# Performance work log

Measured on AMD Instinct MI355X. Metric: run time of the kernel, lower is better.

## Reference

```python
import jax, jax.numpy as jnp
import numpy as np

# ViT-Base-ish encoder: 256x256 img, patch 8 -> N=1024 tokens, dim 768, 8 layers
B, C, H, W = 8, 3, 256, 256
P, D, DEPTH, HEADS, DH, MLP = 8, 768, 8, 12, 64, 3072
N = (H // P) * (W // P)
INNER = HEADS * DH  # 768
EPS = 1e-5


def setup_inputs() -> dict:
    key = jax.random.key(0)
    ks = jax.random.split(key, 8)
    s = lambda i, shape, scale=0.02: jax.random.normal(ks[i], shape, jnp.float32) * scale
    return {
        "x": s(0, (B, C, H, W), 1.0),
        "w_conv": s(1, (D, C, P, P)),          # OIHW conv kernel (patch embed)
        "b_conv": jnp.zeros((D,), jnp.float32),
        "pos_emb": s(2, (1, N, D)),
        "ln1_w": jnp.ones((DEPTH, D), jnp.float32),
        "ln1_b": jnp.zeros((DEPTH, D), jnp.float32),
        "qkv_w": s(3, (DEPTH, D, 3 * INNER)),  # stored [in,out]; Linear has no bias
        "out_w": s(4, (DEPTH, INNER, D)),
        "out_b": jnp.zeros((DEPTH, D), jnp.float32),
        "ln2_w": jnp.ones((DEPTH, D), jnp.float32),
        "ln2_b": jnp.zeros((DEPTH, D), jnp.float32),
        "w1": s(5, (DEPTH, D, MLP)),
        "b1": jnp.zeros((DEPTH, MLP), jnp.float32),
        "w2": s(6, (DEPTH, MLP, D)),
        "b2": jnp.zeros((DEPTH, D), jnp.float32),
    }


def _layernorm(x, w, b):
    m = jnp.mean(x, axis=-1, keepdims=True)
    v = jnp.mean(jnp.square(x - m), axis=-1, keepdims=True)
    return (x - m) * jax.lax.rsqrt(v + EPS) * w + b


def _encoder(x, w_conv, b_conv, pos_emb, ln1_w, ln1_b, qkv_w, out_w, out_b,
             ln2_w, ln2_b, w1, b1, w2, b2):
    # PatchEmbed: strided conv -> flatten(2).transpose(1,2)
    h = jax.lax.conv_general_dilated(
        x, w_conv, window_strides=(P, P), padding='VALID',
        dimension_numbers=('NCHW', 'OIHW', 'NCHW'))
    h = h + b_conv[None, :, None, None]
    h = h.reshape(B, D, N).transpose(0, 2, 1)  # [B, N, D]
    h = h + pos_emb
    scale = DH ** -0.5

    def block(h, p):
        l1w, l1b, qkvw, ow, ob, l2w, l2b, W1, B1, W2, B2 = p
        # PreNorm + MHSA
        y = _layernorm(h, l1w, l1b)
        qkv = y @ qkvw                                   # [B,N,3*INNER]
        q, k, v = jnp.split(qkv, 3, axis=-1)
        split_heads = lambda t: t.reshape(B, N, HEADS, DH).transpose(0, 2, 1, 3)
        q, k, v = split_heads(q), split_heads(k), split_heads(v)
        attn = jax.nn.softmax(jnp.einsum('bhnd,bhmd->bhnm', q, k) * scale, axis=-1)
        o = jnp.einsum('bhnm,bhmd->bhnd', attn, v)
        o = o.transpose(0, 2, 1, 3).reshape(B, N, INNER)
        h = h + (o @ ow + ob)
        # PreNorm + FFN (exact GELU, dropout=0)
        y = _layernorm(h, l2w, l2b)
        h = h + (jax.nn.gelu(y @ W1 + B1, approximate=False) @ W2 + B2)
        return h, None

    h, _ = jax.lax.scan(block, h, (ln1_w, ln1_b, qkv_w, out_w, out_b,
                                   ln2_w, ln2_b, w1, b1, w2, b2))
    return h


def reference(x, w_conv, b_conv, pos_emb, ln1_w, ln1_b, qkv_w, out_w, out_b,
              ln2_w, ln2_b, w1, b1, w2, b2):
    return _encoder(x, w_conv, b_conv, pos_emb, ln1_w, ln1_b, qkv_w, out_w,
                    out_b, ln2_w, ln2_b, w1, b1, w2, b2)
```

## Files before the change

kernel.cpp:

```cpp
#include <hip/hip_runtime.h>
#include <math.h>

#define BATCH 8
#define CIN 3
#define HIMG 256
#define WIMG 256
#define PATCH 8
#define DMODEL 768
#define DEPTH 8
#define HEADS 12
#define DHEAD 64
#define MLPDIM 3072
#define NTOK 1024
#define INNER 768
#define MROWS (BATCH * NTOK)
#define QKVS (3 * INNER)
#define KPATCH (CIN * PATCH * PATCH)
#define LNEPS 1e-5f
#define QSCALE 0.18033688011112042f

typedef __attribute__((ext_vector_type(8))) short short8;
typedef __attribute__((ext_vector_type(4))) float v4f;

__device__ __forceinline__ float b2f(unsigned short u) {
  union { unsigned int i; float f; } x;
  x.i = (unsigned int)u << 16;
  return x.f;
}
__device__ __forceinline__ unsigned short f2b(float f) {
  union { float f; unsigned int i; } x;
  x.f = f;
  unsigned int r = x.i + 0x7FFFu + ((x.i >> 16) & 1u);
  return (unsigned short)(r >> 16);
}
__device__ __forceinline__ unsigned int pkrh(float a, float b) {
  union { float f; unsigned int u; } x, y;
  x.f = a; y.f = b;
  return ((x.u + 0x8000u) >> 16) | ((y.u + 0x8000u) & 0xFFFF0000u);
}

#define GLL(gp, lp)                                                     \
  __builtin_amdgcn_global_load_lds(                                     \
      (const __attribute__((address_space(1))) void*)(gp),              \
      (__attribute__((address_space(3))) void*)(lp), 16, 0, 0)

__global__ __launch_bounds__(256) void cast_kernel(
    const float* __restrict__ src, unsigned short* __restrict__ dst, int n) {
  int i = blockIdx.x * 256 + threadIdx.x;
  if (i < n) dst[i] = f2b(src[i]);
}

__global__ __launch_bounds__(256) void transpose_cast_kernel(
    const float* __restrict__ src, unsigned short* __restrict__ dst, int R,
    int C) {
  __shared__ unsigned short t[32][33];
  src += (size_t)blockIdx.z * R * C;
  dst += (size_t)blockIdx.z * R * C;
  int c0 = blockIdx.x * 32, r0 = blockIdx.y * 32;
  int tx = threadIdx.x & 31, ty = threadIdx.x >> 5;
#pragma unroll
  for (int u = 0; u < 4; ++u) {
    int r = r0 + ty + u * 8;
    t[ty + u * 8][tx] = f2b(src[(size_t)r * C + c0 + tx]);
  }
  __syncthreads();
#pragma unroll
  for (int u = 0; u < 4; ++u) {
    int c = c0 + ty + u * 8;
    dst[(size_t)c * R + r0 + tx] = t[tx][ty + u * 8];
  }
}

__global__ __launch_bounds__(256) void vtrans_kernel(
    const unsigned short* __restrict__ qkv, unsigned short* __restrict__ vt) {
  __shared__ unsigned short t[32][33];
  int k0 = blockIdx.x * 32;
  int d0 = blockIdx.y * 32;
  int bh = blockIdx.z;
  int b = bh / HEADS, h = bh % HEADS;
  int tx = threadIdx.x & 31, ty = threadIdx.x >> 5;
  const unsigned short* src =
      qkv + (size_t)(b * NTOK) * QKVS + 2 * INNER + h * DHEAD;
#pragma unroll
  for (int u = 0; u < 4; ++u)
    t[ty + u * 8][tx] = src[(size_t)(k0 + ty + u * 8) * QKVS + d0 + tx];
  __syncthreads();
  unsigned short* dst = vt + ((size_t)bh * DHEAD + d0) * NTOK + k0;
#pragma unroll
  for (int u = 0; u < 4; ++u)
    dst[(size_t)(ty + u * 8) * NTOK + tx] = t[tx][ty + u * 8];
}

__global__ __launch_bounds__(256) void im2col_kernel(
    const float* __restrict__ x, unsigned short* __restrict__ A) {
  int idx = blockIdx.x * 256 + threadIdx.x;
  if (idx >= MROWS * KPATCH) return;
  int m = idx / KPATCH, k = idx % KPATCH;
  int b = m / NTOK, n = m % NTOK;
  int ph = n / 32, pw = n % 32;
  int c = k / 64, r = k % 64;
  int py = r / 8, px = r % 8;
  A[idx] =
      f2b(x[((size_t)(b * CIN + c) * HIMG + ph * 8 + py) * WIMG + pw * 8 + px]);
}

template <int EPI, int OB, int MT>
__global__ __launch_bounds__(256) void mfma_gemm_kernel(
    const unsigned short* __restrict__ Ag, const unsigned short* __restrict__ Bt,
    const float* __restrict__ bias, const float* __restrict__ res,
    void* __restrict__ Cg, int Mdim, int Ndim, int Kdim) {
  constexpr int MI = MT / 32;
  constexpr int RA = MT / 4;
  constexpr int NCA = RA / 8;
  __shared__ __align__(16) unsigned short Asm[MT * 64];
  __shared__ __align__(16) unsigned short Bsm[128 * 64];
  int tid = threadIdx.x;
  int lane = tid & 63, wv = tid >> 6;

  int Nt = Ndim / 128;
  int mchunk = (Mdim / MT) >> 3;
  int bid = blockIdx.x;
  int xcd = bid & 7;
  int j = bid >> 3;
  int m0 = (xcd * mchunk + j / Nt) * MT;
  int n0 = (j % Nt) * 128;

  v4f acc[MI][4] = {};

  int sr8 = lane >> 3;
  int sc8 = ((lane & 7) ^ sr8) * 8;
  const unsigned short* Aw = Ag + (size_t)(m0 + RA * wv + sr8) * Kdim + sc8;
  const unsigned short* Bw = Bt + (size_t)(n0 + 32 * wv + sr8) * Kdim + sc8;
  unsigned short* As0 = Asm + (RA * wv) * 64;
  unsigned short* Bs0 = Bsm + (32 * wv) * 64;

  int quad = lane >> 4, lr = lane & 15;
  int fr0 = (wv >> 1) * (MI * 16);
  int fc0 = (wv & 1) * 64;
  int xcol = (quad ^ (lr & 7)) * 8;
  const unsigned short* Afr = Asm + (fr0 + lr) * 64;
  const unsigned short* Bfr = Bsm + (fc0 + lr) * 64;

  for (int k0 = 0; k0 < Kdim; k0 += 64) {
#pragma unroll
    for (int c = 0; c < NCA; ++c)
      GLL(Aw + k0 + (size_t)(8 * c) * Kdim, As0 + c * 8 * 64);
#pragma unroll
    for (int c = 0; c < 4; ++c)
      GLL(Bw + k0 + (size_t)(8 * c) * Kdim, Bs0 + c * 8 * 64);
    __syncthreads();
#pragma unroll
    for (int s = 0; s < 2; ++s) {
      int xo = xcol ^ (s * 32);
      short8 af[MI], bf[4];
#pragma unroll
      for (int i = 0; i < MI; ++i)
        af[i] = *(const short8*)(Afr + i * 16 * 64 + xo);
#pragma unroll
      for (int n = 0; n < 4; ++n)
        bf[n] = *(const short8*)(Bfr + n * 16 * 64 + xo);
#pragma unroll
      for (int i = 0; i < MI; ++i)
#pragma unroll
        for (int n = 0; n < 4; ++n)
          acc[i][n] = __builtin_amdgcn_mfma_f32_16x16x32_bf16(
              af[i], bf[n], acc[i][n], 0, 0, 0);
    }
    __syncthreads();
  }

  float* Cf = (float*)Cg;
  unsigned short* Cb = (unsigned short*)Cg;
#pragma unroll
  for (int i = 0; i < MI; ++i) {
#pragma unroll
    for (int n = 0; n < 4; ++n) {
      int ncol = n0 + fc0 + 16 * n + lr;
#pragma unroll
      for (int reg = 0; reg < 4; ++reg) {
        int mrow = m0 + fr0 + 16 * i + quad * 4 + reg;
        float v = acc[i][n][reg];
        if (EPI == 2 || EPI == 3 || EPI == 4) v += bias[ncol];
        if (EPI == 2) v += res[(size_t)mrow * Ndim + ncol];
        if (EPI == 3) {
          float u = v * (0.7978845608028654f + 0.035677408136300125f * v * v);
          float a = fminf(fmaxf(u * 2.8853900817779268f, -60.f), 60.f);
          float E = __builtin_amdgcn_exp2f(a);
          v = v * E * __builtin_amdgcn_rcpf(E + 1.0f);
        }
        if (EPI == 4) v += res[(size_t)(mrow % NTOK) * Ndim + ncol];
        if (EPI == 5 && ncol < INNER) v *= QSCALE;
        if (OB)
          Cb[(size_t)mrow * Ndim + ncol] = f2b(v);
        else
          Cf[(size_t)mrow * Ndim + ncol] = v;
      }
    }
  }
}

#define ABUF8 (256 * 64)
#define BBUF8 (256 * 64)
#define SM8PH (2 * (ABUF8 + BBUF8) * 2)

template <int EPI, int OB>
__global__ __launch_bounds__(512, 2) void gemm8ph_kernel(
    const unsigned short* __restrict__ Ag, const unsigned short* __restrict__ Bt,
    const float* __restrict__ bias, void* __restrict__ Cg, int Mdim, int Ndim,
    int Kdim) {
  extern __shared__ __align__(16) unsigned short sm8[];
  unsigned short* As = sm8;
  unsigned short* Bs = sm8 + 2 * ABUF8;
  int tid = threadIdx.x;
  int lane = tid & 63, wv = tid >> 6;
  int wm = wv >> 2, wn = wv & 3;
  int quad = lane >> 4, lr = lane & 15;

  int Nt = Ndim >> 8;
  int mchunk = (Mdim >> 8) >> 3;
  int bid = blockIdx.x;
  int xcd = bid & 7, j = bid >> 3;
  int m0 = (xcd * mchunk + j / Nt) << 8;
  int n0 = (j % Nt) << 8;
  int NTI = Kdim >> 6;

  int sr8 = lane >> 3;
  int sc8 = ((lane & 7) ^ sr8) * 8;
  const unsigned short* Aw = Ag + (size_t)(m0 + wv * 8 + sr8) * Kdim + sc8;
  const unsigned short* Bw = Bt + (size_t)(n0 + wv * 8 + sr8) * Kdim + sc8;
  unsigned short* AsW = As + (wv * 8) * 64;
  unsigned short* BsW = Bs + (wv * 8) * 64;

  int xq = (quad ^ (lr & 7)) * 8;
  const unsigned short* Afr = As + (wm * 128 + lr) * 64;
  const unsigned short* Bfr = Bs + (wn * 64 + lr) * 64;
  const unsigned short* Afr1 = Afr + ABUF8;
  const unsigned short* Bfr1 = Bfr + BBUF8;

  v4f acc[8][4] = {};
  short8 af[2][4], bf0[2][2], bf1[2][2];

#define STG_A8(buf, tile, half)                                           \
  do {                                                                    \
    GLL(Aw + (size_t)((half) * 128) * Kdim + (tile) * 64,                 \
        AsW + (buf) * ABUF8 + ((half) * 128) * 64);                       \
    GLL(Aw + (size_t)((half) * 128 + 64) * Kdim + (tile) * 64,            \
        AsW + (buf) * ABUF8 + ((half) * 128 + 64) * 64);                  \
  } while (0)
#define STG_B8(buf, tile, half)                                           \
  do {                                                                    \
    GLL(Bw + (size_t)((half) * 128) * Kdim + (tile) * 64,                 \
        BsW + (buf) * BBUF8 + ((half) * 128) * 64);                       \
    GLL(Bw + (size_t)((half) * 128 + 64) * Kdim + (tile) * 64,            \
        BsW + (buf) * BBUF8 + ((half) * 128 + 64) * 64);                  \
  } while (0)

  auto rd_af = [&](const unsigned short* base, int mb) {
#pragma unroll
    for (int s = 0; s < 2; ++s)
#pragma unroll
      for (int m = 0; m < 4; ++m)
        af[s][m] =
            *(const short8*)(base + (mb + m * 16) * 64 + (xq ^ (s * 32)));
  };
  auto rd_bf0 = [&](const unsigned short* base, int nb) {
#pragma unroll
    for (int s = 0; s < 2; ++s)
#pragma unroll
      for (int n = 0; n < 2; ++n)
        bf0[s][n] =
            *(const short8*)(base + (nb + n * 16) * 64 + (xq ^ (s * 32)));
  };
  auto rd_bf1 = [&](const unsigned short* base, int nb) {
#pragma unroll
    for (int s = 0; s < 2; ++s)
#pragma unroll
      for (int n = 0; n < 2; ++n)
        bf1[s][n] =
            *(const short8*)(base + (nb + n * 16) * 64 + (xq ^ (s * 32)));
  };
  auto mfma0 = [&](int mb, int nb) {
#pragma unroll
    for (int s = 0; s < 2; ++s)
#pragma unroll
      for (int m = 0; m < 4; ++m)
#pragma unroll
        for (int n = 0; n < 2; ++n)
          acc[mb + m][nb + n] = __builtin_amdgcn_mfma_f32_16x16x32_bf16(
              af[s][m], bf0[s][n], acc[mb + m][nb + n], 0, 0, 0);
  };
  auto mfma1 = [&](int mb, int nb) {
#pragma unroll
    for (int s = 0; s < 2; ++s)
#pragma unroll
      for (int m = 0; m < 4; ++m)
#pragma unroll
        for (int n = 0; n < 2; ++n)
          acc[mb + m][nb + n] = __builtin_amdgcn_mfma_f32_16x16x32_bf16(
              af[s][m], bf1[s][n], acc[mb + m][nb + n], 0, 0, 0);
  };
  auto mfma_begin = [&]() {
    __builtin_amdgcn_s_barrier();
    asm volatile("s_waitcnt lgkmcnt(0)" ::: "memory");
    __builtin_amdgcn_sched_barrier(0);
    __builtin_amdgcn_s_setprio(1);
  };
  auto mfma_end = [&]() {
    __builtin_amdgcn_s_setprio(0);
    __builtin_amdgcn_s_barrier();
  };

  STG_B8(0, 0, 0);
  STG_B8(0, 0, 1);
  STG_A8(0, 0, 0);
  STG_A8(0, 0, 1);
  STG_B8(1, 1, 0);
  STG_B8(1, 1, 1);
  asm volatile("s_waitcnt vmcnt(4)" ::: "memory");
  __builtin_amdgcn_s_barrier();

  int NI = NTI >> 1;
  for (int i = 0; i < NI; ++i) {
    int t1 = 2 * i + 1, t2 = 2 * i + 2, t3 = 2 * i + 3;
    bool st = t2 < NTI;

    rd_af(Afr, 0);
    rd_bf0(Bfr, 0);
    STG_A8(1, t1, 0);
    mfma_begin();
    mfma0(0, 0);
    mfma_end();
    rd_bf1(Bfr, 32);
    STG_A8(1, t1, 1);
    mfma_begin();
    mfma1(0, 2);
    mfma_end();
    rd_af(Afr, 64);
    if (st) STG_B8(0, t2, 0);
    mfma_begin();
    mfma0(4, 0);
    mfma_end();
    if (st) {
      STG_B8(0, t2, 1);
      asm volatile("s_waitcnt vmcnt(4)" ::: "memory");
    } else {
      asm volatile("s_waitcnt vmcnt(0)" ::: "memory");
    }
    mfma_begin();
    mfma1(4, 2);
    mfma_end();
    rd_af(Afr1, 0);
    rd_bf0(Bfr1, 0);
    if (st) STG_A8(0, t2, 0);
    mfma_begin();
    mfma0(0, 0);
    mfma_end();
    rd_bf1(Bfr1, 32);
    if (st) STG_A8(0, t2, 1);
    mfma_begin();
    mfma1(0, 2);
    mfma_end();
    rd_af(Afr1, 64);
    if (st) STG_B8(1, t3, 0);
    mfma_begin();
    mfma0(4, 0);
    mfma_end();
    if (st) {
      STG_B8(1, t3, 1);
      asm volatile("s_waitcnt vmcnt(4)" ::: "memory");
    }
    mfma_begin();
    mfma1(4, 2);
    mfma_end();
  }
#undef STG_A8
#undef STG_B8

  float* Cf = (float*)Cg;
  unsigned short* Cb = (unsigned short*)Cg;
#pragma unroll
  for (int i = 0; i < 8; ++i) {
#pragma unroll
    for (int n = 0; n < 4; ++n) {
      int ncol = n0 + wn * 64 + 16 * n + lr;
#pragma unroll
      for (int reg = 0; reg < 4; ++reg) {
        int mrow = m0 + wm * 128 + 16 * i + quad * 4 + reg;
        float v = acc[i][n][reg];
        if (EPI == 3) {
          v += bias[ncol];
          float u = v * (0.7978845608028654f + 0.035677408136300125f * v * v);
          float a = fminf(fmaxf(u * 2.8853900817779268f, -60.f), 60.f);
          float E = __builtin_amdgcn_exp2f(a);
          v = v * E * __builtin_amdgcn_rcpf(E + 1.0f);
        }
        if (EPI == 5 && ncol < INNER) v *= QSCALE;
        if (OB)
          Cb[(size_t)mrow * Ndim + ncol] = f2b(v);
        else
          Cf[(size_t)mrow * Ndim + ncol] = v;
      }
    }
  }
}

__global__ __launch_bounds__(256) void ln_kernel(
    const float* __restrict__ x, const float* __restrict__ w,
    const float* __restrict__ b, unsigned short* __restrict__ y) {
  int row = blockIdx.x;
  const float* xr = x + (size_t)row * DMODEL;
  unsigned short* yr = y + (size_t)row * DMODEL;
  int tid = threadIdx.x;
  float v0 = xr[tid], v1 = xr[tid + 256], v2 = xr[tid + 512];
  float s = v0 + v1 + v2;
  __shared__ float red[4];
#pragma unroll
  for (int off = 32; off >= 1; off >>= 1) s += __shfl_xor(s, off, 64);
  if ((tid & 63) == 0) red[tid >> 6] = s;
  __syncthreads();
  float mean = (red[0] + red[1] + red[2] + red[3]) * (1.0f / DMODEL);
  float d0 = v0 - mean, d1 = v1 - mean, d2 = v2 - mean;
  float sq = d0 * d0 + d1 * d1 + d2 * d2;
  __syncthreads();
#pragma unroll
  for (int off = 32; off >= 1; off >>= 1) sq += __shfl_xor(sq, off, 64);
  if ((tid & 63) == 0) red[tid >> 6] = sq;
  __syncthreads();
  float var = (red[0] + red[1] + red[2] + red[3]) * (1.0f / DMODEL);
  float rs = rsqrtf(var + LNEPS);
  yr[tid] = f2b(d0 * rs * w[tid] + b[tid]);
  yr[tid + 256] = f2b(d1 * rs * w[tid + 256] + b[tid + 256]);
  yr[tid + 512] = f2b(d2 * rs * w[tid + 512] + b[tid + 512]);
}

__global__ __launch_bounds__(256) void attn_kernel(
    const unsigned short* __restrict__ qkv,
    const unsigned short* __restrict__ vtg, unsigned short* __restrict__ o) {
  __shared__ __align__(16) unsigned short Ks[64 * 64];
  __shared__ __align__(16) unsigned short Vs[64 * 64];
  __shared__ __align__(16) unsigned short Pl[4][32 * 64];
  int tid = threadIdx.x;
  int lane = tid & 63, wv = tid >> 6;
  int quad = lane >> 4, lr = lane & 15;
  int q0 = blockIdx.x * 128, hh = blockIdx.y, bb = blockIdx.z;

  const unsigned short* qg =
      qkv + (size_t)(bb * NTOK + q0 + wv * 32) * QKVS + hh * DHEAD;
  const unsigned short* kg =
      qkv + (size_t)(bb * NTOK) * QKVS + INNER + hh * DHEAD;
  const unsigned short* vg = vtg + (size_t)(bb * HEADS + hh) * DHEAD * NTOK;
  unsigned short* Pw = Pl[wv];

  int srow = lane >> 3, soff = (lane & 7) * 8;
  int xs = ((lane & 7) ^ srow) * 8;
  int xq = (quad ^ (lr & 7)) * 8;

#pragma unroll
  for (int p = 0; p < 4; ++p) {
    int r = p * 8 + srow;
    *(int4*)(Pw + r * 64 + xs) = *(const int4*)(qg + (size_t)r * QKVS + soff);
  }
  short8 qf[2][2];
#pragma unroll
  for (int n = 0; n < 2; ++n)
#pragma unroll
    for (int s = 0; s < 2; ++s)
      qf[n][s] = *(const short8*)(Pw + (n * 16 + lr) * 64 + (xq ^ (s * 32)));

  v4f oac[2][4] = {};
  float m_i[2] = {-1e30f, -1e30f};
  float l_i[2] = {0.f, 0.f};

  for (int t = 0; t < NTOK / 64; ++t) {
    __syncthreads();
#pragma unroll
    for (int p = 0; p < 2; ++p) {
      int r = wv * 16 + p * 8 + srow;
      *(int4*)(Ks + r * 64 + xs) =
          *(const int4*)(kg + (size_t)(t * 64 + r) * QKVS + soff);
      *(int4*)(Vs + r * 64 + xs) =
          *(const int4*)(vg + (size_t)r * NTOK + t * 64 + soff);
    }
    __syncthreads();

    v4f sac[4][2] = {};
#pragma unroll
    for (int s = 0; s < 2; ++s) {
      short8 kf[4];
#pragma unroll
      for (int mt = 0; mt < 4; ++mt)
        kf[mt] = *(const short8*)(Ks + (mt * 16 + lr) * 64 + (xq ^ (s * 32)));
#pragma unroll
      for (int mt = 0; mt < 4; ++mt)
#pragma unroll
        for (int n = 0; n < 2; ++n)
          sac[mt][n] = __builtin_amdgcn_mfma_f32_16x16x32_bf16(
              kf[mt], qf[n][s], sac[mt][n], 0, 0, 0);
    }

#pragma unroll
    for (int n = 0; n < 2; ++n) {
      float mx = -1e30f;
#pragma unroll
      for (int mt = 0; mt < 4; ++mt)
#pragma unroll
        for (int r = 0; r < 4; ++r) mx = fmaxf(mx, sac[mt][n][r]);
      mx = fmaxf(mx, __shfl_xor(mx, 16, 64));
      mx = fmaxf(mx, __shfl_xor(mx, 32, 64));
      if (!__all(mx - m_i[n] <= 8.0f)) {
        float mnew = fmaxf(m_i[n], mx);
        float alpha = __builtin_amdgcn_exp2f(m_i[n] - mnew);
        m_i[n] = mnew;
        l_i[n] *= alpha;
#pragma unroll
        for (int r = 0; r < 4; ++r) {
          float ao = __shfl(alpha, quad * 4 + r, 64);
#pragma unroll
          for (int j2 = 0; j2 < 4; ++j2) oac[n][j2][r] *= ao;
        }
      }
      float sum = 0.f;
#pragma unroll
      for (int mt = 0; mt < 4; ++mt) {
#pragma unroll
        for (int r = 0; r < 4; ++r) {
          float p = __builtin_amdgcn_exp2f(sac[mt][n][r] - m_i[n]);
          sac[mt][n][r] = p;
          sum += p;
        }
        *(uint2*)(Pw + (n * 16 + lr) * 64 +
                  (((mt * 2 + (quad >> 1)) ^ (lr & 7)) * 8) + (quad & 1) * 4) =
            make_uint2(pkrh(sac[mt][n][0], sac[mt][n][1]),
                       pkrh(sac[mt][n][2], sac[mt][n][3]));
      }
      sum += __shfl_xor(sum, 16, 64);
      sum += __shfl_xor(sum, 32, 64);
      l_i[n] += sum;
    }

#pragma unroll
    for (int s = 0; s < 2; ++s) {
      short8 pf[2], vf[4];
#pragma unroll
      for (int i = 0; i < 2; ++i)
        pf[i] = *(const short8*)(Pw + (i * 16 + lr) * 64 + (xq ^ (s * 32)));
#pragma unroll
      for (int j = 0; j < 4; ++j)
        vf[j] = *(const short8*)(Vs + (j * 16 + lr) * 64 + (xq ^ (s * 32)));
#pragma unroll
      for (int i = 0; i < 2; ++i)
#pragma unroll
        for (int j = 0; j < 4; ++j)
          oac[i][j] = __builtin_amdgcn_mfma_f32_16x16x32_bf16(
              pf[i], vf[j], oac[i][j], 0, 0, 0);
    }
  }

  unsigned short* ob =
      o + (size_t)(bb * NTOK + q0 + wv * 32) * INNER + hh * DHEAD;
#pragma unroll
  for (int i = 0; i < 2; ++i) {
    float inv = 1.0f / l_i[i];
#pragma unroll
    for (int r = 0; r < 4; ++r) {
      float il = __shfl(inv, quad * 4 + r, 64);
      int row = i * 16 + quad * 4 + r;
#pragma unroll
      for (int j = 0; j < 4; ++j)
        ob[(size_t)row * INNER + 16 * j + lr] = f2b(oac[i][j][r] * il);
    }
  }
}

extern "C" void kernel_launch(void* const* d_in, const int* in_sizes, int n_in,
                              void* d_out, int out_size, void* d_ws,
                              size_t ws_size, hipStream_t stream) {
  const float* x      = (const float*)d_in[0];
  const float* w_conv = (const float*)d_in[1];
  const float* b_conv = (const float*)d_in[2];
  const float* pos    = (const float*)d_in[3];
  const float* ln1w   = (const float*)d_in[4];
  const float* ln1b   = (const float*)d_in[5];
  const float* qkvw   = (const float*)d_in[6];
  const float* outw   = (const float*)d_in[7];
  const float* outb   = (const float*)d_in[8];
  const float* ln2w   = (const float*)d_in[9];
  const float* ln2b   = (const float*)d_in[10];
  const float* w1     = (const float*)d_in[11];
  const float* b1     = (const float*)d_in[12];
  const float* w2     = (const float*)d_in[13];
  const float* b2     = (const float*)d_in[14];

  char* ws = (char*)d_ws;
  float* outp = (float*)d_out;
  dim3 blk(256);
  dim3 blk8(512);

  static int use8ph = -1;
  if (use8ph < 0) {
    hipError_t e1 = hipFuncSetAttribute(
        reinterpret_cast<const void*>(&gemm8ph_kernel<5, 1>),
        hipFuncAttributeMaxDynamicSharedMemorySize, SM8PH);
    hipError_t e2 = hipFuncSetAttribute(
        reinterpret_cast<const void*>(&gemm8ph_kernel<3, 1>),
        hipFuncAttributeMaxDynamicSharedMemorySize, SM8PH);
    use8ph = (e1 == hipSuccess && e2 == hipSuccess) ? 1 : 0;
  }

  float* h            = (float*)(ws + 0);
  unsigned short* big = (unsigned short*)(ws + 25165824);
  unsigned short* y   = (unsigned short*)(ws + 75497472);

  const size_t NEEDED = 214204416;
  bool batched = ws_size >= NEEDED;

  unsigned short *vt, *wc, *wqa, *woa, *w1a, *w2a;
  unsigned short *wq_f, *wo_f, *w1_f, *w2_f;
  if (batched) {
    vt  = (unsigned short*)(ws + 88080384);
    wc  = (unsigned short*)(ws + 100663296);
    wqa = (unsigned short*)(ws + 100958208);
    woa = (unsigned short*)(ws + 129269760);
    w1a = (unsigned short*)(ws + 138706944);
    w2a = (unsigned short*)(ws + 176455680);
    wq_f = wo_f = w1_f = w2_f = nullptr;
  } else {
    wq_f = (unsigned short*)(ws + 88080384);
    wo_f = (unsigned short*)(ws + 91619328);
    w1_f = (unsigned short*)(ws + 92798976);
    w2_f = (unsigned short*)(ws + 97517568);
    wc   = (unsigned short*)(ws + 102236160);
    vt   = (unsigned short*)(ws + 102531072);
    wqa = woa = w1a = w2a = nullptr;
  }

  cast_kernel<<<dim3((DMODEL * KPATCH + 255) / 256), blk, 0, stream>>>(
      w_conv, wc, DMODEL * KPATCH);
  im2col_kernel<<<dim3((MROWS * KPATCH + 255) / 256), blk, 0, stream>>>(x, big);
  mfma_gemm_kernel<4, 0, 64>
      <<<dim3((MROWS / 64) * (DMODEL / 128)), blk, 0, stream>>>(
          big, wc, b_conv, pos, h, MROWS, DMODEL, KPATCH);

  if (batched) {
    transpose_cast_kernel<<<dim3(QKVS / 32, DMODEL / 32, DEPTH), blk, 0,
                            stream>>>(qkvw, wqa, DMODEL, QKVS);
    transpose_cast_kernel<<<dim3(DMODEL / 32, INNER / 32, DEPTH), blk, 0,
                            stream>>>(outw, woa, INNER, DMODEL);
    transpose_cast_kernel<<<dim3(MLPDIM / 32, DMODEL / 32, DEPTH), blk, 0,
                            stream>>>(w1, w1a, DMODEL, MLPDIM);
    transpose_cast_kernel<<<dim3(DMODEL / 32, MLPDIM / 32, DEPTH), blk, 0,
                            stream>>>(w2, w2a, MLPDIM, DMODEL);
  }

  for (int l = 0; l < DEPTH; ++l) {
    unsigned short* wq = batched ? wqa + (size_t)l * DMODEL * QKVS : wq_f;
    unsigned short* wo = batched ? woa + (size_t)l * INNER * DMODEL : wo_f;
    unsigned short* w1t = batched ? w1a + (size_t)l * DMODEL * MLPDIM : w1_f;
    unsigned short* w2t = batched ? w2a + (size_t)l * MLPDIM * DMODEL : w2_f;
    if (!batched) {
      transpose_cast_kernel<<<dim3(QKVS / 32, DMODEL / 32), blk, 0, stream>>>(
          qkvw + (size_t)l * DMODEL * QKVS, wq, DMODEL, QKVS);
    }
    ln_kernel<<<dim3(MROWS), blk, 0, stream>>>(h, ln1w + l * DMODEL,
                                               ln1b + l * DMODEL, y);
    if (use8ph)
      gemm8ph_kernel<5, 1>
          <<<dim3((MROWS / 256) * (QKVS / 256)), blk8, SM8PH, stream>>>(
              y, wq, nullptr, big, MROWS, QKVS, DMODEL);
    else
      mfma_gemm_kernel<5, 1, 128>
          <<<dim3((MROWS / 128) * (QKVS / 128)), blk, 0, stream>>>(
              y, wq, nullptr, nullptr, big, MROWS, QKVS, DMODEL);
    vtrans_kernel<<<dim3(NTOK / 32, DHEAD / 32, BATCH * HEADS), blk, 0,
                    stream>>>(big, vt);
    attn_kernel<<<dim3(NTOK / 128, HEADS, BATCH), blk, 0, stream>>>(big, vt, y);
    if (!batched) {
      transpose_cast_kernel<<<dim3(DMODEL / 32, INNER / 32), blk, 0, stream>>>(
          outw + (size_t)l * INNER * DMODEL, wo, INNER, DMODEL);
    }
    mfma_gemm_kernel<2, 0, 64>
        <<<dim3((MROWS / 64) * (DMODEL / 128)), blk, 0, stream>>>(
            y, wo, outb + l * DMODEL, h, h, MROWS, DMODEL, INNER);
    ln_kernel<<<dim3(MROWS), blk, 0, stream>>>(h, ln2w + l * DMODEL,
                                               ln2b + l * DMODEL, y);
    if (!batched) {
      transpose_cast_kernel<<<dim3(MLPDIM / 32, DMODEL / 32), blk, 0, stream>>>(
          w1 + (size_t)l * DMODEL * MLPDIM, w1t, DMODEL, MLPDIM);
    }
    if (use8ph)
      gemm8ph_kernel<3, 1>
          <<<dim3((MROWS / 256) * (MLPDIM / 256)), blk8, SM8PH, stream>>>(
              y, w1t, b1 + l * MLPDIM, big, MROWS, MLPDIM, DMODEL);
    else
      mfma_gemm_kernel<3, 1, 128>
          <<<dim3((MROWS / 128) * (MLPDIM / 128)), blk, 0, stream>>>(
              y, w1t, b1 + l * MLPDIM, nullptr, big, MROWS, MLPDIM, DMODEL);
    if (!batched) {
      transpose_cast_kernel<<<dim3(DMODEL / 32, MLPDIM / 32), blk, 0, stream>>>(
          w2 + (size_t)l * MLPDIM * DMODEL, w2t, MLPDIM, DMODEL);
    }
    float* dst = (l == DEPTH - 1) ? outp : h;
    mfma_gemm_kernel<2, 0, 64>
        <<<dim3((MROWS / 64) * (DMODEL / 128)), blk, 0, stream>>>(
            big, w2t, b2 + l * DMODEL, h, dst, MROWS, DMODEL, MLPDIM);
  }
}
```

Measured before the change: 2.326 ms.

## Double-buffer K/V tiles with async global-to-LDS loads and XCD-aware block mapping

The attention kernel now keeps two K/V tile buffers in shared memory. It issues direct global-to-LDS loads (the GLL helper) for the next 64-key tile while computing on the current one, which hides load latency and removes one barrier per iteration. The launch grid is flattened to 1D and block ids are remapped so that all query blocks of the same (batch, head) land on the same XCD, which should improve L2 reuse of K/V. In exchange the kernel uses more LDS, which may cut occupancy, and it depends on the swizzle being correct under the GLL lane-address layout.

```diff
diff --git a/kernel.cpp b/kernel.cpp
--- a/kernel.cpp
+++ b/kernel.cpp
@@ -436,13 +436,18 @@
 __global__ __launch_bounds__(256) void attn_kernel(
     const unsigned short* __restrict__ qkv,
     const unsigned short* __restrict__ vtg, unsigned short* __restrict__ o) {
-  __shared__ __align__(16) unsigned short Ks[64 * 64];
-  __shared__ __align__(16) unsigned short Vs[64 * 64];
+  __shared__ __align__(16) unsigned short Ks[2][64 * 64];
+  __shared__ __align__(16) unsigned short Vs[2][64 * 64];
   __shared__ __align__(16) unsigned short Pl[4][32 * 64];
   int tid = threadIdx.x;
   int lane = tid & 63, wv = tid >> 6;
   int quad = lane >> 4, lr = lane & 15;
-  int q0 = blockIdx.x * 128, hh = blockIdx.y, bb = blockIdx.z;
+
+  int bid = blockIdx.x;
+  int xcd = bid & 7, j = bid >> 3;
+  int hl = xcd * 12 + (j % 12);
+  int qb = j / 12;
+  int q0 = qb * 128, hh = hl % HEADS, bb = hl / HEADS;
 
   const unsigned short* qg =
       qkv + (size_t)(bb * NTOK + q0 + wv * 32) * QKVS + hh * DHEAD;
@@ -455,6 +460,17 @@
   int xs = ((lane & 7) ^ srow) * 8;
   int xq = (quad ^ (lr & 7)) * 8;
 
+#define STG_KV(buf, t)                                                    \
+  do {                                                                    \
+    _Pragma("unroll") for (int p = 0; p < 2; ++p) {                       \
+      int rr = wv * 16 + p * 8;                                           \
+      GLL(kg + (size_t)((t) * 64 + rr + srow) * QKVS + xs,                \
+          &Ks[buf][rr * 64]);                                             \
+      GLL(vg + (size_t)(rr + srow) * NTOK + (t) * 64 + xs,                \
+          &Vs[buf][rr * 64]);                                             \
+    }                                                                     \
+  } while (0)
+
 #pragma unroll
   for (int p = 0; p < 4; ++p) {
     int r = p * 8 + srow;
@@ -471,17 +487,15 @@
   float m_i[2] = {-1e30f, -1e30f};
   float l_i[2] = {0.f, 0.f};
 
+  STG_KV(0, 0);
+  asm volatile("s_waitcnt vmcnt(0)" ::: "memory");
+  __syncthreads();
+
+  int cur = 0;
   for (int t = 0; t < NTOK / 64; ++t) {
-    __syncthreads();
-#pragma unroll
-    for (int p = 0; p < 2; ++p) {
-      int r = wv * 16 + p * 8 + srow;
-      *(int4*)(Ks + r * 64 + xs) =
-          *(const int4*)(kg + (size_t)(t * 64 + r) * QKVS + soff);
-      *(int4*)(Vs + r * 64 + xs) =
-          *(const int4*)(vg + (size_t)r * NTOK + t * 64 + soff);
-    }
-    __syncthreads();
+    if (t < NTOK / 64 - 1) STG_KV(cur ^ 1, t + 1);
+    const unsigned short* Kc = Ks[cur];
+    const unsigned short* Vc = Vs[cur];
 
     v4f sac[4][2] = {};
 #pragma unroll
@@ -489,7 +503,7 @@
       short8 kf[4];
 #pragma unroll
       for (int mt = 0; mt < 4; ++mt)
-        kf[mt] = *(const short8*)(Ks + (mt * 16 + lr) * 64 + (xq ^ (s * 32)));
+        kf[mt] = *(const short8*)(Kc + (mt * 16 + lr) * 64 + (xq ^ (s * 32)));
 #pragma unroll
       for (int mt = 0; mt < 4; ++mt)
 #pragma unroll
@@ -545,16 +559,21 @@
       for (int i = 0; i < 2; ++i)
         pf[i] = *(const short8*)(Pw + (i * 16 + lr) * 64 + (xq ^ (s * 32)));
 #pragma unroll
-      for (int j = 0; j < 4; ++j)
-        vf[j] = *(const short8*)(Vs + (j * 16 + lr) * 64 + (xq ^ (s * 32)));
+      for (int j2 = 0; j2 < 4; ++j2)
+        vf[j2] = *(const short8*)(Vc + (j2 * 16 + lr) * 64 + (xq ^ (s * 32)));
 #pragma unroll
       for (int i = 0; i < 2; ++i)
 #pragma unroll
-        for (int j = 0; j < 4; ++j)
-          oac[i][j] = __builtin_amdgcn_mfma_f32_16x16x32_bf16(
-              pf[i], vf[j], oac[i][j], 0, 0, 0);
-    }
-  }
+        for (int j2 = 0; j2 < 4; ++j2)
+          oac[i][j2] = __builtin_amdgcn_mfma_f32_16x16x32_bf16(
+              pf[i], vf[j2], oac[i][j2], 0, 0, 0);
+    }
+
+    asm volatile("s_waitcnt vmcnt(0)" ::: "memory");
+    __syncthreads();
+    cur ^= 1;
+  }
+#undef STG_KV
 
   unsigned short* ob =
       o + (size_t)(bb * NTOK + q0 + wv * 32) * INNER + hh * DHEAD;
@@ -566,8 +585,8 @@
       float il = __shfl(inv, quad * 4 + r, 64);
       int row = i * 16 + quad * 4 + r;
 #pragma unroll
-      for (int j = 0; j < 4; ++j)
-        ob[(size_t)row * INNER + 16 * j + lr] = f2b(oac[i][j][r] * il);
+      for (int j2 = 0; j2 < 4; ++j2)
+        ob[(size_t)row * INNER + 16 * j2 + lr] = f2b(oac[i][j2][r] * il);
     }
   }
 }
@@ -673,7 +692,8 @@
               y, wq, nullptr, nullptr, big, MROWS, QKVS, DMODEL);
     vtrans_kernel<<<dim3(NTOK / 32, DHEAD / 32, BATCH * HEADS), blk, 0,
                     stream>>>(big, vt);
-    attn_kernel<<<dim3(NTOK / 128, HEADS, BATCH), blk, 0, stream>>>(big, vt, y);
+    attn_kernel<<<dim3((NTOK / 128) * HEADS * BATCH), blk, 0, stream>>>(
+        big, vt, y);
     if (!batched) {
       transpose_cast_kernel<<<dim3(DMODEL / 32, INNER / 32), blk, 0, stream>>>(
           outw + (size_t)l * INNER * DMODEL, wo, INNER, DMODEL);
```

After: 2.306 ms. Within noise of the previous version (-0.9%).
